# Performance work log

Hardware: AMD Instinct MI355X
Metric: run time of the kernel (lower is better)

## Reference

```python
import jax, jax.numpy as jnp
import numpy as np

HEADS = 8
DIM_HEAD = 64
LN_EPS = 1e-5


def rotate_half(x):
    # pairs (x0,x1) -> (-x1,x0), interleaved layout (einops '(d r)' with r=2)
    x1 = x[..., 0::2]
    x2 = x[..., 1::2]
    return jnp.stack((-x2, x1), axis=-1).reshape(x.shape)


def apply_rope(freqs, x):
    return x * jnp.cos(freqs) + rotate_half(x) * jnp.sin(freqs)


def setup_inputs() -> dict:
    key = jax.random.key(0)
    ks = jax.random.split(key, 4)
    b, n, dim = 2, 4096, 512
    inner = HEADS * DIM_HEAD
    x = jax.random.normal(ks[0], (b, n, dim), dtype=jnp.float32)
    rotary_time_emb = jax.random.uniform(ks[1], (b, n, DIM_HEAD), jnp.float32, 0.0, 6.283185)
    ln_w = jnp.ones((dim,), jnp.float32)
    ln_b = jnp.zeros((dim,), jnp.float32)
    w_qkv = jax.random.normal(ks[2], (inner * 3, dim), jnp.float32) * (dim ** -0.5)
    w_out = jax.random.normal(ks[3], (dim, inner), jnp.float32) * (inner ** -0.5)
    b_out = jnp.zeros((dim,), jnp.float32)
    return dict(x=x, rotary_time_emb=rotary_time_emb, ln_w=ln_w, ln_b=ln_b,
                w_qkv=w_qkv, w_out=w_out, b_out=b_out)


def reference(x, rotary_time_emb, ln_w, ln_b, w_qkv, w_out, b_out):
    b, n, dim = x.shape
    # LayerNorm
    mu = jnp.mean(x, axis=-1, keepdims=True)
    var = jnp.var(x, axis=-1, keepdims=True)
    xn = (x - mu) * jax.lax.rsqrt(var + LN_EPS) * ln_w + ln_b
    # QKV projection (Linear, no bias)
    qkv = xn @ w_qkv.T  # [b, n, 3*inner]
    q, k, v = jnp.split(qkv, 3, axis=-1)

    def to_heads(t):
        return t.reshape(b, n, HEADS, DIM_HEAD).transpose(0, 2, 1, 3)  # b h n d

    q, k, v = to_heads(q), to_heads(k), to_heads(v)
    freqs = rotary_time_emb[:, None, :, :]  # b 1 n d, broadcast over heads
    q = apply_rope(freqs, q)
    k = apply_rope(freqs, k)
    v = apply_rope(freqs, v)  # rotate_value=True
    scale = jnp.asarray(DIM_HEAD ** -0.5, dtype=x.dtype)
    scores = jnp.einsum('bhqd,bhkd->bhqk', q, k) * scale
    attn = jax.nn.softmax(scores, axis=-1)
    out = jnp.einsum('bhqk,bhkd->bhqd', attn, v)
    out = apply_rope(-freqs, out)  # inverse rotation of the output
    out = out.transpose(0, 2, 1, 3).reshape(b, n, HEADS * DIM_HEAD)
    return out @ w_out.T + b_out
```

## Files before the change

kernel.cpp:

```cpp
#include <hip/hip_runtime.h>
#include <cmath>

typedef short bf16x8 __attribute__((ext_vector_type(8)));
typedef float f32x2 __attribute__((ext_vector_type(2)));
typedef float f32x4 __attribute__((ext_vector_type(4)));
typedef float f32x16 __attribute__((ext_vector_type(16)));

#define NSEQ 4096
#define BATCH 2
#define DIM 512
#define HEADS 8
#define NROWS (BATCH * NSEQ)
#define QKVN (3 * DIM)

__device__ __forceinline__ unsigned short f2bf(float f) {
  unsigned int u = __float_as_uint(f);
  u += 0x7fffu + ((u >> 16) & 1u);
  return (unsigned short)(u >> 16);
}
__device__ __forceinline__ float bf2f(unsigned short h) {
  return __uint_as_float(((unsigned int)h) << 16);
}
__device__ __forceinline__ void gload16(const unsigned short* g, unsigned short* l) {
  __builtin_amdgcn_global_load_lds((const __attribute__((address_space(1))) unsigned int*)g,
                                   (__attribute__((address_space(3))) unsigned int*)l, 16, 0, 0);
}

__global__ __launch_bounds__(256) void k_tables(const float* __restrict__ rot,
                                                float* __restrict__ cosT,
                                                float* __restrict__ sinT) {
  int i = blockIdx.x * 256 + threadIdx.x;
  float f = rot[i];
  cosT[i] = cosf(f);
  sinT[i] = sinf(f);
}

__global__ __launch_bounds__(256) void k_cvt(const float* __restrict__ src,
                                             unsigned short* __restrict__ dst, int n) {
  int i = blockIdx.x * 256 + threadIdx.x;
  if (i < n) dst[i] = f2bf(src[i]);
}

__global__ __launch_bounds__(256) void k_ln(const float* __restrict__ x,
                                            const float* __restrict__ w,
                                            const float* __restrict__ bb,
                                            unsigned short* __restrict__ xn) {
  int row = blockIdx.x * 4 + (threadIdx.x >> 6);
  int lane = threadIdx.x & 63;
  const float* xr = x + (size_t)row * DIM;
  float v[8];
  float s = 0.f;
#pragma unroll
  for (int j = 0; j < 8; ++j) { v[j] = xr[lane + j * 64]; s += v[j]; }
#pragma unroll
  for (int m = 1; m < 64; m <<= 1) s += __shfl_xor(s, m);
  float mu = s * (1.0f / DIM);
  float q = 0.f;
#pragma unroll
  for (int j = 0; j < 8; ++j) { float d = v[j] - mu; q += d * d; }
#pragma unroll
  for (int m = 1; m < 64; m <<= 1) q += __shfl_xor(q, m);
  float rs = rsqrtf(q * (1.0f / DIM) + 1e-5f);
#pragma unroll
  for (int j = 0; j < 8; ++j) {
    int col = lane + j * 64;
    xn[(size_t)row * DIM + col] = f2bf((v[j] - mu) * rs * w[col] + bb[col]);
  }
}

template <int EPI>
__global__ __launch_bounds__(256) void k_gemm(const unsigned short* __restrict__ A,
                                              const unsigned short* __restrict__ B,
                                              void* __restrict__ C,
                                              const float* __restrict__ bias,
                                              int M, int N, int K) {
  __shared__ __align__(16) unsigned short As[2][128 * 32];
  __shared__ __align__(16) unsigned short Bs[2][128 * 32];
  int bm = blockIdx.x, bn = blockIdx.y;
  int tid = threadIdx.x;
  int lane = tid & 63, w = tid >> 6;
  int wm = (w >> 1) << 6, wn = (w & 1) << 6;
  f32x4 acc[4][4] = {};

#define GSTAGE(KT, BUF) do { \
  _Pragma("unroll") \
  for (int i = 0; i < 2; ++i) { \
    int c = tid + (i << 8); \
    int row = c >> 2, kc = (c & 3) << 3; \
    gload16(A + (size_t)(bm * 128 + row) * K + (KT) + kc, &As[BUF][(w * 64 + i * 256) * 8]); \
    gload16(B + (size_t)(bn * 128 + row) * K + (KT) + kc, &Bs[BUF][(w * 64 + i * 256) * 8]); \
  } } while (0)

  GSTAGE(0, 0);
  __syncthreads();
  int nk = K >> 5;
  for (int t = 0; t < nk; ++t) {
    int cur = t & 1;
    if (t + 1 < nk) GSTAGE((t + 1) << 5, cur ^ 1);
    bf16x8 af[4], bfr[4];
#pragma unroll
    for (int mi = 0; mi < 4; ++mi)
      af[mi] = *(const bf16x8*)&As[cur][(wm + mi * 16 + (lane & 15)) * 32 + ((lane >> 4) << 3)];
#pragma unroll
    for (int ni = 0; ni < 4; ++ni)
      bfr[ni] = *(const bf16x8*)&Bs[cur][(wn + ni * 16 + (lane & 15)) * 32 + ((lane >> 4) << 3)];
#pragma unroll
    for (int mi = 0; mi < 4; ++mi)
#pragma unroll
      for (int ni = 0; ni < 4; ++ni)
        acc[mi][ni] = __builtin_amdgcn_mfma_f32_16x16x32_bf16(af[mi], bfr[ni], acc[mi][ni], 0, 0, 0);
    __syncthreads();
  }
#undef GSTAGE
#pragma unroll
  for (int mi = 0; mi < 4; ++mi) {
#pragma unroll
    for (int ni = 0; ni < 4; ++ni) {
#pragma unroll
      for (int r = 0; r < 4; ++r) {
        int gm = bm * 128 + wm + mi * 16 + ((lane >> 4) << 2) + r;
        int gn = bn * 128 + wn + ni * 16 + (lane & 15);
        if (EPI == 0) {
          ((unsigned short*)C)[(size_t)gm * N + gn] = f2bf(acc[mi][ni][r]);
        } else {
          ((float*)C)[(size_t)gm * N + gn] = acc[mi][ni][r] + bias[gn];
        }
      }
    }
  }
}

__global__ __launch_bounds__(256) void k_rope_split(const unsigned short* __restrict__ qkv,
                                                    const float* __restrict__ cosT,
                                                    const float* __restrict__ sinT,
                                                    unsigned short* __restrict__ qh,
                                                    unsigned short* __restrict__ kh,
                                                    unsigned short* __restrict__ vt) {
  __shared__ unsigned short vs[128][65];
  const float QSC = 0.125f * 1.44269504f;
  int nt = blockIdx.x, bh = blockIdx.y;
  int b = bh >> 3, h = bh & 7;
  int n0 = nt * 128;
  int t = threadIdx.x;
  int sub = t >> 3, cc = t & 7;
#pragma unroll
  for (int rr = 0; rr < 4; ++rr) {
    int row = rr * 32 + sub;
    int n = n0 + row;
    size_t base = ((size_t)(b * NSEQ + n)) * QKVN + h * 64 + cc * 8;
    const float* cb = cosT + ((size_t)(b * NSEQ + n)) * 64 + cc * 8;
    const float* sb = sinT + ((size_t)(b * NSEQ + n)) * 64 + cc * 8;
    float c[8], sn[8];
#pragma unroll
    for (int j = 0; j < 8; ++j) { c[j] = cb[j]; sn[j] = sb[j]; }
    bf16x8 qv = *(const bf16x8*)(qkv + base);
    bf16x8 kv = *(const bf16x8*)(qkv + base + 512);
    bf16x8 vv = *(const bf16x8*)(qkv + base + 1024);
    union { bf16x8 v; unsigned short u[8]; } yq, yk;
#pragma unroll
    for (int j = 0; j < 8; j += 2) {
      {
        float e = bf2f((unsigned short)qv[j]), o = bf2f((unsigned short)qv[j + 1]);
        yq.u[j]     = f2bf((e * c[j] - o * sn[j]) * QSC);
        yq.u[j + 1] = f2bf((o * c[j + 1] + e * sn[j + 1]) * QSC);
      }
      {
        float e = bf2f((unsigned short)kv[j]), o = bf2f((unsigned short)kv[j + 1]);
        yk.u[j]     = f2bf(e * c[j] - o * sn[j]);
        yk.u[j + 1] = f2bf(o * c[j + 1] + e * sn[j + 1]);
      }
      {
        float e = bf2f((unsigned short)vv[j]), o = bf2f((unsigned short)vv[j + 1]);
        vs[row][cc * 8 + j]     = f2bf(e * c[j] - o * sn[j]);
        vs[row][cc * 8 + j + 1] = f2bf(o * c[j + 1] + e * sn[j + 1]);
      }
    }
    *(bf16x8*)(qh + ((size_t)bh * NSEQ + n) * 64 + cc * 8) = yq.v;
    *(bf16x8*)(kh + ((size_t)bh * NSEQ + n) * 64 + cc * 8) = yk.v;
  }
  __syncthreads();
  int d = t >> 2, c4 = t & 3;
#pragma unroll
  for (int g = 0; g < 4; ++g) {
    union { bf16x8 v; unsigned short u[8]; } tv;
#pragma unroll
    for (int j = 0; j < 8; ++j) tv.u[j] = vs[c4 * 32 + g * 8 + j][d];
    *(bf16x8*)(vt + ((size_t)bh * 64 + d) * NSEQ + n0 + c4 * 32 + g * 8) = tv.v;
  }
}

__global__ __launch_bounds__(256, 2) void k_attn(const unsigned short* __restrict__ Qh,
                                                 const unsigned short* __restrict__ Kh,
                                                 const unsigned short* __restrict__ VT,
                                                 float* __restrict__ opart,
                                                 float* __restrict__ lpart) {
  __shared__ __align__(16) unsigned short Ks[4][64 * 64];
  __shared__ __align__(16) unsigned short Vs[4][64 * 64];
  int bid = blockIdx.x;
  int bh   = (bid & 7) + 8 * ((bid >> 7) & 1);
  int qt   = (bid >> 3) & 15;
  int half = (bid >> 8) & 1;
  int tid = threadIdx.x;
  int w = tid >> 6, lane = tid & 63;
  int lq = lane & 31, hi = lane >> 5;
  int q0 = qt * 256 + w * 64;
  int kv0 = half * 2048;

  const unsigned short* Kbh = Kh + (size_t)bh * NSEQ * 64;
  const unsigned short* Vbh = VT + (size_t)bh * 64 * NSEQ;

  const unsigned short* QbA = Qh + ((size_t)bh * NSEQ + q0 + lq) * 64 + hi * 8;
  const unsigned short* QbB = QbA + 32 * 64;
  bf16x8 qfA[4], qfB[4];
#pragma unroll
  for (int j = 0; j < 4; ++j) {
    qfA[j] = *(const bf16x8*)(QbA + j * 16);
    qfB[j] = *(const bf16x8*)(QbB + j * 16);
  }

  int c0 = w * 64 + lane;
  int r0 = c0 >> 3, sw0 = ((c0 & 7) ^ (r0 & 7)) << 3;
  int c1 = c0 + 256;
  int r1 = c1 >> 3, sw1 = ((c1 & 7) ^ (r1 & 7)) << 3;
  int ld0 = (w * 64) * 8, ld1 = (256 + w * 64) * 8;

  f32x16 accA0 = (f32x16)0.0f, accA1 = (f32x16)0.0f;
  f32x16 accB0 = (f32x16)0.0f, accB1 = (f32x16)0.0f;
  float lA = 0.f, lB = 0.f;
  int swz = (lq & 7) << 4;

#define STAGE(T, BUF) do { \
  int tg_ = kv0 + (T) * 64; \
  gload16(Kbh + ((size_t)tg_ + r0) * 64 + sw0, &Ks[BUF][ld0]); \
  gload16(Kbh + ((size_t)tg_ + r1) * 64 + sw1, &Ks[BUF][ld1]); \
  gload16(Vbh + (size_t)r0 * NSEQ + tg_ + sw0, &Vs[BUF][ld0]); \
  gload16(Vbh + (size_t)r1 * NSEQ + tg_ + sw1, &Vs[BUF][ld1]); \
} while (0)

  STAGE(0, 0);
  STAGE(1, 1);

  for (int t = 0; t < 32; ++t) {
    int rd = t & 3;
    if (t < 30) {
      STAGE(t + 2, (t + 2) & 3);
      asm volatile("s_waitcnt vmcnt(8)" ::: "memory");
    } else if (t == 30) {
      asm volatile("s_waitcnt vmcnt(4)" ::: "memory");
    } else {
      asm volatile("s_waitcnt vmcnt(0)" ::: "memory");
    }
    __builtin_amdgcn_s_barrier();
    asm volatile("" ::: "memory");
    const char* kb_ = (const char*)&Ks[rd][0];
    const char* vb_ = (const char*)&Vs[rd][0];
#pragma unroll
    for (int ph = 0; ph < 2; ++ph) {
      f32x16 sA = (f32x16)0.0f, sB = (f32x16)0.0f;
      __builtin_amdgcn_s_setprio(1);
#pragma unroll
      for (int j = 0; j < 4; ++j) {
        int cb = j * 32 + hi * 16;
        bf16x8 a = *(const bf16x8*)(kb_ + (ph * 32 + lq) * 128 + (cb ^ swz));
        sA = __builtin_amdgcn_mfma_f32_32x32x16_bf16(a, qfA[j], sA, 0, 0, 0);
        sB = __builtin_amdgcn_mfma_f32_32x32x16_bf16(a, qfB[j], sB, 0, 0, 0);
      }
      __builtin_amdgcn_s_setprio(0);
#pragma unroll
      for (int r = 0; r < 16; ++r) sA[r] = __builtin_amdgcn_exp2f(sA[r]);
#pragma unroll
      for (int r = 0; r < 16; ++r) sB[r] = __builtin_amdgcn_exp2f(sB[r]);
      {
        union { f32x16 v; f32x2 p[8]; } ua, ub; ua.v = sA; ub.v = sB;
        f32x2 a01 = ua.p[0] + ua.p[1], a23 = ua.p[2] + ua.p[3];
        f32x2 a45 = ua.p[4] + ua.p[5], a67 = ua.p[6] + ua.p[7];
        f32x2 ta = (a01 + a23) + (a45 + a67);
        lA += ta.x + ta.y;
        f32x2 b01 = ub.p[0] + ub.p[1], b23 = ub.p[2] + ub.p[3];
        f32x2 b45 = ub.p[4] + ub.p[5], b67 = ub.p[6] + ub.p[7];
        f32x2 tb = (b01 + b23) + (b45 + b67);
        lB += tb.x + tb.y;
      }
      unsigned int dwA[8], dwB[8];
#pragma unroll
      for (int m = 0; m < 8; ++m) {
        asm("v_cvt_pk_bf16_f32 %0, %1, %2" : "=v"(dwA[m]) : "v"(sA[2 * m]), "v"(sA[2 * m + 1]));
        asm("v_cvt_pk_bf16_f32 %0, %1, %2" : "=v"(dwB[m]) : "v"(sB[2 * m]), "v"(sB[2 * m + 1]));
      }
      __builtin_amdgcn_s_setprio(1);
#pragma unroll
      for (int kk = 0; kk < 2; ++kk) {
        const int B = 4 * kk;
        unsigned int svA0 = hi ? dwA[B + 0] : dwA[B + 2];
        unsigned int svA1 = hi ? dwA[B + 1] : dwA[B + 3];
        unsigned int svB0 = hi ? dwB[B + 0] : dwB[B + 2];
        unsigned int svB1 = hi ? dwB[B + 1] : dwB[B + 3];
        unsigned int rvA0 = (unsigned int)__shfl_xor((int)svA0, 32);
        unsigned int rvA1 = (unsigned int)__shfl_xor((int)svA1, 32);
        unsigned int rvB0 = (unsigned int)__shfl_xor((int)svB0, 32);
        unsigned int rvB1 = (unsigned int)__shfl_xor((int)svB1, 32);
        union { unsigned int d[4]; bf16x8 v; } puA, puB;
        puA.d[0] = hi ? rvA0 : dwA[B + 0];
        puA.d[1] = hi ? rvA1 : dwA[B + 1];
        puA.d[2] = hi ? dwA[B + 2] : rvA0;
        puA.d[3] = hi ? dwA[B + 3] : rvA1;
        puB.d[0] = hi ? rvB0 : dwB[B + 0];
        puB.d[1] = hi ? rvB1 : dwB[B + 1];
        puB.d[2] = hi ? dwB[B + 2] : rvB0;
        puB.d[3] = hi ? dwB[B + 3] : rvB1;
        int cb = (ph * 2 + kk) * 32 + hi * 16;
        bf16x8 v0 = *(const bf16x8*)(vb_ + lq * 128 + (cb ^ swz));
        bf16x8 v1 = *(const bf16x8*)(vb_ + (32 + lq) * 128 + (cb ^ swz));
        accA0 = __builtin_amdgcn_mfma_f32_32x32x16_bf16(v0, puA.v, accA0, 0, 0, 0);
        accA1 = __builtin_amdgcn_mfma_f32_32x32x16_bf16(v1, puA.v, accA1, 0, 0, 0);
        accB0 = __builtin_amdgcn_mfma_f32_32x32x16_bf16(v0, puB.v, accB0, 0, 0, 0);
        accB1 = __builtin_amdgcn_mfma_f32_32x32x16_bf16(v1, puB.v, accB1, 0, 0, 0);
      }
      __builtin_amdgcn_s_setprio(0);
    }
  }
#undef STAGE

  float lsumA = lA + __shfl_xor(lA, 32);
  float lsumB = lB + __shfl_xor(lB, 32);
  size_t qrowA = (size_t)(half * 16 + bh) * NSEQ + q0 + lq;
  size_t qrowB = qrowA + 32;
  if (hi == 0) {
    lpart[qrowA] = lsumA;
    lpart[qrowB] = lsumB;
  }
  float* obA = opart + qrowA * 64;
  float* obB = opart + qrowB * 64;
#pragma unroll
  for (int rg = 0; rg < 4; ++rg) {
    float4 a0 = make_float4(accA0[4 * rg + 0], accA0[4 * rg + 1], accA0[4 * rg + 2], accA0[4 * rg + 3]);
    float4 a1 = make_float4(accA1[4 * rg + 0], accA1[4 * rg + 1], accA1[4 * rg + 2], accA1[4 * rg + 3]);
    float4 b0 = make_float4(accB0[4 * rg + 0], accB0[4 * rg + 1], accB0[4 * rg + 2], accB0[4 * rg + 3]);
    float4 b1 = make_float4(accB1[4 * rg + 0], accB1[4 * rg + 1], accB1[4 * rg + 2], accB1[4 * rg + 3]);
    *(float4*)(obA + 8 * rg + 4 * hi) = a0;
    *(float4*)(obA + 32 + 8 * rg + 4 * hi) = a1;
    *(float4*)(obB + 8 * rg + 4 * hi) = b0;
    *(float4*)(obB + 32 + 8 * rg + 4 * hi) = b1;
  }
}

__global__ __launch_bounds__(256) void k_combine(const float* __restrict__ opart,
                                                 const float* __restrict__ lpart,
                                                 const float* __restrict__ cosT,
                                                 const float* __restrict__ sinT,
                                                 unsigned short* __restrict__ ao) {
  int bh = blockIdx.y;
  int b = bh >> 3, h = bh & 7;
  int t = threadIdx.x;
  int q = blockIdx.x * 16 + (t >> 4);
  int d = (t & 15) * 4;
  size_t i0 = (size_t)bh * NSEQ + q;
  const size_t HOFF = (size_t)16 * NSEQ;
  float4 o0 = *(const float4*)(opart + i0 * 64 + d);
  float4 o1 = *(const float4*)(opart + (i0 + HOFF) * 64 + d);
  float inv = 1.0f / (lpart[i0] + lpart[i0 + HOFF]);
  float4 c4 = *(const float4*)(cosT + ((size_t)b * NSEQ + q) * 64 + d);
  float4 s4 = *(const float4*)(sinT + ((size_t)b * NSEQ + q) * 64 + d);
  float yx = (o0.x + o1.x) * inv;
  float yy = (o0.y + o1.y) * inv;
  float yz = (o0.z + o1.z) * inv;
  float yw = (o0.w + o1.w) * inv;
  float r0 = yx * c4.x + yy * s4.x;
  float r1 = yy * c4.y - yx * s4.y;
  float r2 = yz * c4.z + yw * s4.z;
  float r3 = yw * c4.w - yz * s4.w;
  unsigned int w0, w1;
  asm("v_cvt_pk_bf16_f32 %0, %1, %2" : "=v"(w0) : "v"(r0), "v"(r1));
  asm("v_cvt_pk_bf16_f32 %0, %1, %2" : "=v"(w1) : "v"(r2), "v"(r3));
  unsigned int uu[2] = {w0, w1};
  *(uint2*)(ao + ((size_t)b * NSEQ + q) * DIM + h * 64 + d) = *(uint2*)uu;
}

extern "C" void kernel_launch(void* const* d_in, const int* in_sizes, int n_in,
                              void* d_out, int out_size, void* d_ws, size_t ws_size,
                              hipStream_t stream) {
  const float* x    = (const float*)d_in[0];
  const float* rot  = (const float*)d_in[1];
  const float* lnw  = (const float*)d_in[2];
  const float* lnb  = (const float*)d_in[3];
  const float* wqkv = (const float*)d_in[4];
  const float* wout = (const float*)d_in[5];
  const float* bout = (const float*)d_in[6];
  float* out = (float*)d_out;

  char* ws = (char*)d_ws;
  const size_t MB = (size_t)1 << 20;
  float* cosT          = (float*)(ws + 0 * MB);
  float* sinT          = (float*)(ws + 2 * MB);
  unsigned short* wqkb = (unsigned short*)(ws + 4 * MB);
  float* lpart         = (float*)(ws + 5 * MB + 512 * 1024);
  unsigned short* wob  = (unsigned short*)(ws + 6 * MB);
  unsigned short* xn   = (unsigned short*)(ws + 8 * MB);
  float* opart         = (float*)(ws + 8 * MB);
  unsigned short* qkv  = (unsigned short*)(ws + 16 * MB);
  unsigned short* qh   = (unsigned short*)(ws + 40 * MB);
  unsigned short* ao   = (unsigned short*)(ws + 40 * MB);
  unsigned short* kh   = (unsigned short*)(ws + 48 * MB);
  unsigned short* vt   = (unsigned short*)(ws + 56 * MB);

  k_tables<<<(BATCH * NSEQ * 64) / 256, 256, 0, stream>>>(rot, cosT, sinT);
  k_cvt<<<(QKVN * DIM + 255) / 256, 256, 0, stream>>>(wqkv, wqkb, QKVN * DIM);
  k_cvt<<<(DIM * DIM + 255) / 256, 256, 0, stream>>>(wout, wob, DIM * DIM);
  k_ln<<<NROWS / 4, 256, 0, stream>>>(x, lnw, lnb, xn);
  k_gemm<0><<<dim3(NROWS / 128, QKVN / 128), 256, 0, stream>>>(xn, wqkb, qkv, nullptr,
                                                               NROWS, QKVN, DIM);
  k_rope_split<<<dim3(NSEQ / 128, 16), 256, 0, stream>>>(qkv, cosT, sinT, qh, kh, vt);
  k_attn<<<512, 256, 0, stream>>>(qh, kh, vt, opart, lpart);
  k_combine<<<dim3(NSEQ / 16, 16), 256, 0, stream>>>(opart, lpart, cosT, sinT, ao);
  k_gemm<1><<<dim3(NROWS / 128, DIM / 128), 256, 0, stream>>>(ao, wob, out, bout,
                                                              NROWS, DIM, DIM);
}
```

Before: 147.4 us.

## Merge prep kernels, store attention partials in bf16, stagger LDS phase per wave

Three launches (the cos/sin table build and the two weight conversions) are merged into one k_prep kernel that dispatches on block index, which removes launch overhead. The split-KV attention partial outputs are now written as bf16 instead of fp32 and widened back in k_combine, halving that intermediate traffic. Waves 2-3 process the two 32-row K halves in swapped order, likely to spread LDS bank access. Rounding the unnormalized partials to bf16 before combining adds some precision loss.

```diff
diff --git a/kernel.cpp b/kernel.cpp
--- a/kernel.cpp
+++ b/kernel.cpp
@@ -26,19 +26,27 @@
                                    (__attribute__((address_space(3))) unsigned int*)l, 16, 0, 0);
 }
 
-__global__ __launch_bounds__(256) void k_tables(const float* __restrict__ rot,
-                                                float* __restrict__ cosT,
-                                                float* __restrict__ sinT) {
-  int i = blockIdx.x * 256 + threadIdx.x;
-  float f = rot[i];
-  cosT[i] = cosf(f);
-  sinT[i] = sinf(f);
-}
-
-__global__ __launch_bounds__(256) void k_cvt(const float* __restrict__ src,
-                                             unsigned short* __restrict__ dst, int n) {
-  int i = blockIdx.x * 256 + threadIdx.x;
-  if (i < n) dst[i] = f2bf(src[i]);
+__global__ __launch_bounds__(256) void k_prep(const float* __restrict__ rot,
+                                              float* __restrict__ cosT,
+                                              float* __restrict__ sinT,
+                                              const float* __restrict__ wqkv,
+                                              unsigned short* __restrict__ wqkb,
+                                              const float* __restrict__ wout,
+                                              unsigned short* __restrict__ wob) {
+  int bid = blockIdx.x;
+  int t = threadIdx.x;
+  if (bid < 2048) {
+    int i = bid * 256 + t;
+    float f = rot[i];
+    cosT[i] = cosf(f);
+    sinT[i] = sinf(f);
+  } else if (bid < 5120) {
+    int i = (bid - 2048) * 256 + t;
+    wqkb[i] = f2bf(wqkv[i]);
+  } else {
+    int i = (bid - 5120) * 256 + t;
+    wob[i] = f2bf(wout[i]);
+  }
 }
 
 __global__ __launch_bounds__(256) void k_ln(const float* __restrict__ x,
@@ -192,7 +200,7 @@
 __global__ __launch_bounds__(256, 2) void k_attn(const unsigned short* __restrict__ Qh,
                                                  const unsigned short* __restrict__ Kh,
                                                  const unsigned short* __restrict__ VT,
-                                                 float* __restrict__ opart,
+                                                 unsigned short* __restrict__ opart,
                                                  float* __restrict__ lpart) {
   __shared__ __align__(16) unsigned short Ks[4][64 * 64];
   __shared__ __align__(16) unsigned short Vs[4][64 * 64];
@@ -205,6 +213,7 @@
   int lq = lane & 31, hi = lane >> 5;
   int q0 = qt * 256 + w * 64;
   int kv0 = half * 2048;
+  int pswap = w >> 1;
 
   const unsigned short* Kbh = Kh + (size_t)bh * NSEQ * 64;
   const unsigned short* Vbh = VT + (size_t)bh * 64 * NSEQ;
@@ -255,7 +264,8 @@
     const char* kb_ = (const char*)&Ks[rd][0];
     const char* vb_ = (const char*)&Vs[rd][0];
 #pragma unroll
-    for (int ph = 0; ph < 2; ++ph) {
+    for (int pp = 0; pp < 2; ++pp) {
+      int ph = pp ^ pswap;
       f32x16 sA = (f32x16)0.0f, sB = (f32x16)0.0f;
       __builtin_amdgcn_s_setprio(1);
 #pragma unroll
@@ -329,22 +339,27 @@
     lpart[qrowA] = lsumA;
     lpart[qrowB] = lsumB;
   }
-  float* obA = opart + qrowA * 64;
-  float* obB = opart + qrowB * 64;
+  unsigned short* obA = opart + qrowA * 64;
+  unsigned short* obB = opart + qrowB * 64;
 #pragma unroll
   for (int rg = 0; rg < 4; ++rg) {
-    float4 a0 = make_float4(accA0[4 * rg + 0], accA0[4 * rg + 1], accA0[4 * rg + 2], accA0[4 * rg + 3]);
-    float4 a1 = make_float4(accA1[4 * rg + 0], accA1[4 * rg + 1], accA1[4 * rg + 2], accA1[4 * rg + 3]);
-    float4 b0 = make_float4(accB0[4 * rg + 0], accB0[4 * rg + 1], accB0[4 * rg + 2], accB0[4 * rg + 3]);
-    float4 b1 = make_float4(accB1[4 * rg + 0], accB1[4 * rg + 1], accB1[4 * rg + 2], accB1[4 * rg + 3]);
-    *(float4*)(obA + 8 * rg + 4 * hi) = a0;
-    *(float4*)(obA + 32 + 8 * rg + 4 * hi) = a1;
-    *(float4*)(obB + 8 * rg + 4 * hi) = b0;
-    *(float4*)(obB + 32 + 8 * rg + 4 * hi) = b1;
-  }
-}
-
-__global__ __launch_bounds__(256) void k_combine(const float* __restrict__ opart,
+    unsigned int pa0[2], pa1[2], pb0[2], pb1[2];
+    asm("v_cvt_pk_bf16_f32 %0, %1, %2" : "=v"(pa0[0]) : "v"(accA0[4 * rg + 0]), "v"(accA0[4 * rg + 1]));
+    asm("v_cvt_pk_bf16_f32 %0, %1, %2" : "=v"(pa0[1]) : "v"(accA0[4 * rg + 2]), "v"(accA0[4 * rg + 3]));
+    asm("v_cvt_pk_bf16_f32 %0, %1, %2" : "=v"(pa1[0]) : "v"(accA1[4 * rg + 0]), "v"(accA1[4 * rg + 1]));
+    asm("v_cvt_pk_bf16_f32 %0, %1, %2" : "=v"(pa1[1]) : "v"(accA1[4 * rg + 2]), "v"(accA1[4 * rg + 3]));
+    asm("v_cvt_pk_bf16_f32 %0, %1, %2" : "=v"(pb0[0]) : "v"(accB0[4 * rg + 0]), "v"(accB0[4 * rg + 1]));
+    asm("v_cvt_pk_bf16_f32 %0, %1, %2" : "=v"(pb0[1]) : "v"(accB0[4 * rg + 2]), "v"(accB0[4 * rg + 3]));
+    asm("v_cvt_pk_bf16_f32 %0, %1, %2" : "=v"(pb1[0]) : "v"(accB1[4 * rg + 0]), "v"(accB1[4 * rg + 1]));
+    asm("v_cvt_pk_bf16_f32 %0, %1, %2" : "=v"(pb1[1]) : "v"(accB1[4 * rg + 2]), "v"(accB1[4 * rg + 3]));
+    *(uint2*)(obA + 8 * rg + 4 * hi) = *(uint2*)pa0;
+    *(uint2*)(obA + 32 + 8 * rg + 4 * hi) = *(uint2*)pa1;
+    *(uint2*)(obB + 8 * rg + 4 * hi) = *(uint2*)pb0;
+    *(uint2*)(obB + 32 + 8 * rg + 4 * hi) = *(uint2*)pb1;
+  }
+}
+
+__global__ __launch_bounds__(256) void k_combine(const unsigned short* __restrict__ opart,
                                                  const float* __restrict__ lpart,
                                                  const float* __restrict__ cosT,
                                                  const float* __restrict__ sinT,
@@ -356,15 +371,23 @@
   int d = (t & 15) * 4;
   size_t i0 = (size_t)bh * NSEQ + q;
   const size_t HOFF = (size_t)16 * NSEQ;
-  float4 o0 = *(const float4*)(opart + i0 * 64 + d);
-  float4 o1 = *(const float4*)(opart + (i0 + HOFF) * 64 + d);
-  float inv = 1.0f / (lpart[i0] + lpart[i0 + HOFF]);
+  float l = lpart[i0] + lpart[i0 + HOFF];
+  float o[4] = {0.f, 0.f, 0.f, 0.f};
+#pragma unroll
+  for (int p = 0; p < 2; ++p) {
+    uint2 u = *(const uint2*)(opart + (i0 + p * HOFF) * 64 + d);
+    o[0] += bf2f((unsigned short)(u.x & 0xffff));
+    o[1] += bf2f((unsigned short)(u.x >> 16));
+    o[2] += bf2f((unsigned short)(u.y & 0xffff));
+    o[3] += bf2f((unsigned short)(u.y >> 16));
+  }
+  float inv = 1.0f / l;
   float4 c4 = *(const float4*)(cosT + ((size_t)b * NSEQ + q) * 64 + d);
   float4 s4 = *(const float4*)(sinT + ((size_t)b * NSEQ + q) * 64 + d);
-  float yx = (o0.x + o1.x) * inv;
-  float yy = (o0.y + o1.y) * inv;
-  float yz = (o0.z + o1.z) * inv;
-  float yw = (o0.w + o1.w) * inv;
+  float yx = o[0] * inv;
+  float yy = o[1] * inv;
+  float yz = o[2] * inv;
+  float yw = o[3] * inv;
   float r0 = yx * c4.x + yy * s4.x;
   float r1 = yy * c4.y - yx * s4.y;
   float r2 = yz * c4.z + yw * s4.z;
@@ -396,16 +419,14 @@
   float* lpart         = (float*)(ws + 5 * MB + 512 * 1024);
   unsigned short* wob  = (unsigned short*)(ws + 6 * MB);
   unsigned short* xn   = (unsigned short*)(ws + 8 * MB);
-  float* opart         = (float*)(ws + 8 * MB);
+  unsigned short* opart = (unsigned short*)(ws + 8 * MB);
   unsigned short* qkv  = (unsigned short*)(ws + 16 * MB);
   unsigned short* qh   = (unsigned short*)(ws + 40 * MB);
   unsigned short* ao   = (unsigned short*)(ws + 40 * MB);
   unsigned short* kh   = (unsigned short*)(ws + 48 * MB);
   unsigned short* vt   = (unsigned short*)(ws + 56 * MB);
 
-  k_tables<<<(BATCH * NSEQ * 64) / 256, 256, 0, stream>>>(rot, cosT, sinT);
-  k_cvt<<<(QKVN * DIM + 255) / 256, 256, 0, stream>>>(wqkv, wqkb, QKVN * DIM);
-  k_cvt<<<(DIM * DIM + 255) / 256, 256, 0, stream>>>(wout, wob, DIM * DIM);
+  k_prep<<<6144, 256, 0, stream>>>(rot, cosT, sinT, wqkv, wqkb, wout, wob);
   k_ln<<<NROWS / 4, 256, 0, stream>>>(x, lnw, lnb, xn);
   k_gemm<0><<<dim3(NROWS / 128, QKVN / 128), 256, 0, stream>>>(xn, wqkb, qkv, nullptr,
                                                                NROWS, QKVN, DIM);
```

Result: faster. 141.0 us (-4.3%).
